# Optimization experiments

Measured on AMD Instinct MI355X. Metric: run time of the kernel, lower is better.

The kernel has to match this reference:

```python
import jax, jax.numpy as jnp
import numpy as np

K = 4
TEMPERATURE = 34.0
OUT_CH = 256
KSIZE = 3
PAD = 1


def setup_inputs() -> dict:
    key = jax.random.key(0)
    ks = jax.random.split(key, 6)
    B, C, H, W = 16, 256, 56, 56
    hidden = int(C * 0.25) + 1  # 65
    x = jax.random.normal(ks[0], (B, C, H, W), dtype=jnp.float32)
    w_fc1 = jax.random.normal(ks[1], (hidden, C), dtype=jnp.float32) * (2.0 / C) ** 0.5
    w_fc2 = jax.random.normal(ks[2], (K, hidden), dtype=jnp.float32) * (2.0 / hidden) ** 0.5
    b_fc2 = jnp.zeros((K,), dtype=jnp.float32)
    weight = jax.random.normal(ks[3], (OUT_CH, C, KSIZE, KSIZE), dtype=jnp.float32) * 0.05
    bias = jax.random.normal(ks[4], (K, OUT_CH), dtype=jnp.float32) * 0.01
    return {"x": x, "w_fc1": w_fc1, "w_fc2": w_fc2, "b_fc2": b_fc2,
            "weight": weight, "bias": bias}


def _attention(x, w_fc1, w_fc2, b_fc2):
    pooled = x.mean(axis=(2, 3))                     # [B, C] adaptive avgpool(1)
    h = jax.nn.relu(pooled @ w_fc1.T)                # 1x1 conv == linear
    raw = h @ w_fc2.T + b_fc2                        # [B, K]
    # gradient_approximation: hard one-hot fwd, softmax(x/T) bwd (straight-through)
    hard = jax.nn.one_hot(jnp.argmax(raw, axis=1), raw.shape[1], dtype=raw.dtype)
    soft = jax.nn.softmax(raw / TEMPERATURE, axis=1)
    att = jax.lax.stop_gradient(hard - soft) + soft
    return att, raw


def _quantize_banks(weight):
    # WDoReFaQuantizer with 'modified' scheme, bits 2..K+1, STE on the round step
    w = weight.reshape(-1)
    t = jnp.tanh(w)
    xq = t / jnp.max(jnp.abs(t))
    xq = (xq + 1.0) * 0.5                            # in [0, 1]
    banks = []
    for bit in range(2, 2 + K):
        a = float(1 << bit)
        q = jnp.minimum(jnp.floor(a * xq), a - 1.0) / a
        q = jax.lax.stop_gradient(q - xq) + xq       # STE: identity backward
        banks.append(q * 2.0 - 1.0)
    return jnp.stack(banks)                          # [K, O*C*k*k]


def reference(x, w_fc1, w_fc2, b_fc2, weight, bias):
    B, C, H, W = x.shape
    att, raw = _attention(x, w_fc1, w_fc2, b_fc2)    # [B, K], [B, K]
    wq = _quantize_banks(weight)                     # [K, N]
    agg_w = (att @ wq).reshape(B, OUT_CH, C, KSIZE, KSIZE)
    agg_b = att @ bias                               # [B, OUT_CH]

    def conv1(xi, wi):  # xi: [C,H,W], wi: [O,C,k,k]
        return jax.lax.conv_general_dilated(
            xi[None], wi, window_strides=(1, 1),
            padding=[(PAD, PAD), (PAD, PAD)],
            dimension_numbers=("NCHW", "OIHW", "NCHW"))[0]

    out = jax.vmap(conv1)(x, agg_w) + agg_b[:, :, None, None]
    return (out, raw)
```

## Files before the change

kernel.cpp:

```cpp
#include <hip/hip_runtime.h>
#include <math.h>

#define NB 16
#define NC 256
#define NH 56
#define NW 56
#define NHW 3136
#define NHID 65
#define NK 4
#define NOC 256
#define WN 589824
#define OUT0 12845056

#define WS_POOLED 0
#define WS_KB     4096
#define WS_MAX    4112
#define WS_MAXP   4128
#define WS_WQF    8192
#define WQB_OFF   32768ul
#define XP_OFF    4751360ul
#define WS_NEED   32325632ul

typedef unsigned int u32;
typedef unsigned short u16;
typedef unsigned long long u64;
typedef __attribute__((ext_vector_type(8))) short s8v;
typedef __attribute__((ext_vector_type(16))) float f16v;

__device__ __forceinline__ u16 f2bf(float f) {
    union { float f; u32 u; } v; v.f = f;
    u32 u = v.u;
    return (u16)((u + 0x7fffu + ((u >> 16) & 1u)) >> 16);
}

__device__ __forceinline__ void gload_lds16(const void* g, void* l) {
    __builtin_amdgcn_global_load_lds((const __attribute__((address_space(1))) u32*)g,
                                     (__attribute__((address_space(3))) u32*)l, 16, 0, 0);
}


__global__ __launch_bounds__(256) void k_prep(const float* __restrict__ x,
                                              const float* __restrict__ w,
                                              float* __restrict__ ws,
                                              float* __restrict__ scratch) {
    const int tid = threadIdx.x;
    if (blockIdx.x >= 896) {
        int j = blockIdx.x - 896;
        float m = 0.f;
        for (int i = j * 256 + tid; i < WN; i += 65536)
            m = fmaxf(m, fabsf(tanhf(w[i])));
        for (int off = 32; off > 0; off >>= 1) m = fmaxf(m, __shfl_down(m, off, 64));
        __shared__ float part[4];
        int lane = tid & 63, wv = tid >> 6;
        if (lane == 0) part[wv] = m;
        __syncthreads();
        if (tid == 0)
            ws[WS_MAXP + j] = fmaxf(fmaxf(part[0], part[1]), fmaxf(part[2], part[3]));
        return;
    }
    const int by = blockIdx.x;
    const int b = by / 56, y = by % 56;
    const int c16 = tid >> 4, q = tid & 15;
    __shared__ __align__(8) u16 Lbt[56 * 264];
    __shared__ float pl[256];
    u16* xp = (u16*)((char*)ws + XP_OFF);

    #pragma unroll
    for (int ci = 0; ci < 16; ++ci) {
        int c = ci * 16 + c16;
        float4 v = make_float4(0.f, 0.f, 0.f, 0.f);
        if (q < 14) {
            v = *(const float4*)(x + ((size_t)(b * 256 + c)) * NHW + (size_t)y * 56 + q * 4);
            Lbt[(q * 4 + 0) * 264 + c] = f2bf(v.x);
            Lbt[(q * 4 + 1) * 264 + c] = f2bf(v.y);
            Lbt[(q * 4 + 2) * 264 + c] = f2bf(v.z);
            Lbt[(q * 4 + 3) * 264 + c] = f2bf(v.w);
        }
        float s = v.x + v.y + v.z + v.w;
        s += __shfl_down(s, 8, 16);
        s += __shfl_down(s, 4, 16);
        s += __shfl_down(s, 2, 16);
        s += __shfl_down(s, 1, 16);
        if (q == 0) pl[c] = s;
    }
    __syncthreads();
    scratch[(size_t)by * 256 + tid] = pl[tid];
    u64* rowp = (u64*)xp + (size_t)(b * 58 + y + 1) * (58 * 64);
    for (int idx = tid; idx < 58 * 64; idx += 256) {
        int col = idx >> 6, cp = idx & 63;
        u64 v = 0ull;
        if (col >= 1 && col <= 56)
            v = *(const u64*)(Lbt + (col - 1) * 264 + cp * 4);
        rowp[idx] = v;
    }
    if (y == 0 || y == 55) {
        int row = (y == 0) ? 0 : 57;
        u64* brow = (u64*)xp + (size_t)(b * 58 + row) * (58 * 64);
        for (int idx = tid; idx < 58 * 64; idx += 256) brow[idx] = 0ull;
    }
}

__global__ __launch_bounds__(256) void k_mid(const float* __restrict__ w_fc1,
                                             const float* __restrict__ w_fc2,
                                             const float* __restrict__ b_fc2,
                                             const float* __restrict__ w,
                                             float* __restrict__ ws,
                                             const float* __restrict__ scratch,
                                             float* __restrict__ out_raw) {
    const int tid = threadIdx.x;
    if (blockIdx.x < 16) {
        const int b = blockIdx.x;
        __shared__ float pl[NC];
        __shared__ float hs[NHID];
        __shared__ float raws[NK];
        float p = 0.f;
        for (int y = 0; y < 56; ++y)
            p += scratch[((size_t)(b * 56 + y)) * 256 + tid];
        pl[tid] = p * (1.0f / NHW);
        __syncthreads();
        if (tid < NHID) {
            float s = 0.f;
            for (int c = 0; c < NC; ++c) s = fmaf(pl[c], w_fc1[tid * NC + c], s);
            hs[tid] = fmaxf(s, 0.f);
        }
        __syncthreads();
        if (tid < NK) {
            float s = b_fc2[tid];
            for (int j = 0; j < NHID; ++j) s = fmaf(hs[j], w_fc2[tid * NHID + j], s);
            raws[tid] = s;
            out_raw[b * NK + tid] = s;
        }
        __syncthreads();
        if (tid == 0) {
            int best = 0;
            for (int k = 1; k < NK; ++k) if (raws[k] > raws[best]) best = k;
            ((int*)(ws + WS_KB))[b] = best;
        }
        return;
    }
    __shared__ float mred[4];
    float mv = ws[WS_MAXP + tid];
    for (int off = 32; off > 0; off >>= 1) mv = fmaxf(mv, __shfl_down(mv, off, 64));
    if ((tid & 63) == 0) mred[tid >> 6] = mv;
    __syncthreads();
    const float maxt = fmaxf(fmaxf(mred[0], mred[1]), fmaxf(mred[2], mred[3]));

    u16* wqp = (u16*)((char*)ws + WQB_OFF);
    int idx = (blockIdx.x - 16) * 256 + tid;
    int o = idx >> 7, c2 = idx & 127;
    int ch0 = c2 * 2;
    int cs = ch0 >> 5, cc = ch0 & 31;
    int ks2 = cc >> 4, hf = (cc >> 3) & 1, j = cc & 7;
    int n = o & 31, ot = o >> 5;
    const float* wp = w + ((size_t)o * 256 + ch0) * 9;
    float t0[9], t1[9];
    #pragma unroll
    for (int t = 0; t < 9; ++t) t0[t] = tanhf(wp[t]);
    #pragma unroll
    for (int t = 0; t < 9; ++t) t1[t] = tanhf(wp[9 + t]);
    #pragma unroll
    for (int bank = 0; bank < 4; ++bank) {
        float a = (float)(4 << bank);
        #pragma unroll
        for (int tap = 0; tap < 9; ++tap) {
            float xq0 = (t0[tap] / maxt + 1.f) * 0.5f;
            float xq1 = (t1[tap] / maxt + 1.f) * 0.5f;
            float q0 = fminf(floorf(a * xq0), a - 1.f) / a * 2.f - 1.f;
            float q1 = fminf(floorf(a * xq1), a - 1.f) / a * 2.f - 1.f;
            u32 pk = (u32)f2bf(q0) | ((u32)f2bf(q1) << 16);
            size_t off16 = ((((size_t)((bank * 8 + ot) * 8 + cs)) * 18 + tap * 2 + ks2) * 64
                            + hf * 32 + n) * 8 + j;
            *(u32*)(wqp + off16) = pk;
        }
    }
}

__global__ __launch_bounds__(256, 2) void k_conv_mfma(const float* __restrict__ bias,
                                                      const float* __restrict__ ws_f,
                                                      float* __restrict__ out) {
    const int L = blockIdx.x;
    const int xcd = L & 7, slot = L >> 3;
    const int oq = slot >> 4;
    const int pair = xcd * 16 + (slot & 15);
    const int b = pair >> 3, strip = pair & 7;
    const int r0 = strip * 7;
    const int tid = threadIdx.x;
    const int wv = tid >> 6, lane = tid & 63;
    const int n = lane & 31, hf = lane >> 5;
    const int vw = (wv + (slot & 3)) & 3;
    const int nt = (vw == 0) ? 4 : 3;
    const int t0 = (vw == 0) ? 0 : 4 + (vw - 1) * 3;
    const int kb = ((const int*)(ws_f + WS_KB))[b];
    const u16* wqp = (const u16*)((const char*)ws_f + WQB_OFF);
    const u16* xp  = (const u16*)((const char*)ws_f + XP_OFF);

    __shared__ __align__(16) u16 Xl[2][9216];
    __shared__ __align__(16) u16 Al[2][9216];

    int bofs[4];
    #pragma unroll
    for (int t = 0; t < 4; ++t) {
        int p = (t0 + t) * 32 + n;
        if (t >= nt || p > 391) p = 391;
        int pr = p / 56, pc = p - pr * 56;
        bofs[t] = pr * 2048 + hf * 1024 + pc * 16;
    }
    const int colc = (lane < 58) ? lane : 57;
    const u16* xsrc = xp + (((size_t)(b * 58 + r0)) * 58 + colc) * 256;
    const u16* ab0 = wqp + (size_t)((kb * 8 + oq * 2 + 0) * 8) * (18 * 64 * 8);
    const u16* ab1 = wqp + (size_t)((kb * 8 + oq * 2 + 1) * 8) * (18 * 64 * 8);

    f16v acc0[4], acc1[4];
    #pragma unroll
    for (int t = 0; t < 4; ++t) { acc0[t] = (f16v)0.f; acc1[t] = (f16v)0.f; }

#define STAGE(stn, bn)                                                                   \
    {                                                                                    \
        const int csn = (stn) >> 1, ksn = (stn) & 1;                                     \
        _Pragma("unroll")                                                                \
        for (int i = 0; i < 9; ++i) {                                                    \
            int seg = wv * 9 + i;                                                        \
            if (seg < 18) {                                                              \
                gload_lds16(xsrc + (size_t)(seg >> 1) * (58 * 256) + (stn) * 16 + (seg & 1) * 8, \
                            (void*)(&Xl[bn][seg * 512]));                                \
            } else {                                                                     \
                int aa = seg - 18;                                                       \
                int tile = (aa >= 9) ? 1 : 0;                                            \
                int tap = aa - tile * 9;                                                 \
                const u16* ab = tile ? ab1 : ab0;                                        \
                gload_lds16(ab + (size_t)(csn * 18 + tap * 2 + ksn) * 512 + lane * 8,    \
                            (void*)(&Al[bn][aa * 512]));                                 \
            }                                                                            \
        }                                                                                \
    }

    STAGE(0, 0);

    #pragma unroll 1
    for (int st = 0; st < 16; ++st) {
        int pb = st & 1;
        if (st < 15) {
            STAGE(st + 1, pb ^ 1);
            asm volatile("s_waitcnt vmcnt(9)" ::: "memory");
        } else {
            asm volatile("s_waitcnt vmcnt(0)" ::: "memory");
        }
        __builtin_amdgcn_s_barrier();
        __builtin_amdgcn_s_setprio(1);
        const u16* AB = &Al[pb][0];
        const char* XB = (const char*)&Xl[pb][0];
        #pragma unroll
        for (int tap = 0; tap < 9; ++tap) {
            s8v a0 = *(const s8v*)(AB + tap * 512 + lane * 8);
            s8v a1 = *(const s8v*)(AB + (9 + tap) * 512 + lane * 8);
            const int r = tap / 3, s = tap % 3;
            const int coff = r * 2048 + s * 16;
            #pragma unroll
            for (int t = 0; t < 4; ++t)
                if (t < nt) {
                    s8v bf = *(const s8v*)(XB + bofs[t] + coff);
                    acc0[t] = __builtin_amdgcn_mfma_f32_32x32x16_bf16(a0, bf, acc0[t], 0, 0, 0);
                    acc1[t] = __builtin_amdgcn_mfma_f32_32x32x16_bf16(a1, bf, acc1[t], 0, 0, 0);
                }
        }
        __builtin_amdgcn_s_setprio(0);
        asm volatile("" ::: "memory");
        __builtin_amdgcn_s_barrier();
    }
#undef STAGE

    #pragma unroll
    for (int t = 0; t < 4; ++t)
        if (t < nt) {
            int p = (t0 + t) * 32 + n;
            if (p < 392) {
                int pr = p / 56, pc = p - pr * 56;
                float* op = out + (size_t)b * 256 * NHW + (size_t)(r0 + pr) * 56 + pc;
                #pragma unroll
                for (int reg = 0; reg < 16; ++reg) {
                    int m = (reg & 3) + 8 * (reg >> 2) + 4 * hf;
                    int o0 = oq * 64 + m;
                    op[(size_t)o0 * NHW] = acc0[t][reg] + bias[kb * NOC + o0];
                    op[(size_t)(o0 + 32) * NHW] = acc1[t][reg] + bias[kb * NOC + o0 + 32];
                }
            }
        }
}


__global__ __launch_bounds__(256) void k_pool(const float* __restrict__ x,
                                              float* __restrict__ ws) {
    int plane = blockIdx.x;
    const float* p = x + (size_t)plane * NHW;
    float s = 0.f;
    for (int i = threadIdx.x; i < NHW; i += 256) s += p[i];
    for (int off = 32; off > 0; off >>= 1) s += __shfl_down(s, off, 64);
    __shared__ float part[4];
    int lane = threadIdx.x & 63, wv = threadIdx.x >> 6;
    if (lane == 0) part[wv] = s;
    __syncthreads();
    if (threadIdx.x == 0)
        ws[WS_POOLED + plane] = part[0] + part[1] + part[2] + part[3];
}

__global__ __launch_bounds__(256) void k_fc(const float* __restrict__ w_fc1,
                                            const float* __restrict__ w_fc2,
                                            const float* __restrict__ b_fc2,
                                            float* __restrict__ ws,
                                            float* __restrict__ out_raw) {
    __shared__ float pl[NB * NC];
    __shared__ float hs[NB][NHID];
    __shared__ float raws[NB][NK];
    for (int i = threadIdx.x; i < NB * NC; i += 256)
        pl[i] = ws[WS_POOLED + i] * (1.0f / NHW);
    __syncthreads();
    for (int idx = threadIdx.x; idx < NB * NHID; idx += 256) {
        int b = idx / NHID, j = idx % NHID;
        float s = 0.f;
        for (int c = 0; c < NC; ++c) s = fmaf(pl[b * NC + c], w_fc1[j * NC + c], s);
        hs[b][j] = fmaxf(s, 0.f);
    }
    __syncthreads();
    if (threadIdx.x < NB * NK) {
        int b = threadIdx.x / NK, k = threadIdx.x % NK;
        float s = b_fc2[k];
        for (int j = 0; j < NHID; ++j) s = fmaf(hs[b][j], w_fc2[k * NHID + j], s);
        raws[b][k] = s;
        out_raw[b * NK + k] = s;
    }
    __syncthreads();
    if (threadIdx.x < NB) {
        int best = 0;
        for (int k = 1; k < NK; ++k)
            if (raws[threadIdx.x][k] > raws[threadIdx.x][best]) best = k;
        ((int*)(ws + WS_KB))[threadIdx.x] = best;
    }
}

__global__ __launch_bounds__(256) void k_maxtanh(const float* __restrict__ w,
                                                 float* __restrict__ ws) {
    float m = 0.f;
    for (int i = blockIdx.x * 256 + threadIdx.x; i < WN; i += gridDim.x * 256)
        m = fmaxf(m, fabsf(tanhf(w[i])));
    for (int off = 32; off > 0; off >>= 1) m = fmaxf(m, __shfl_down(m, off, 64));
    __shared__ float part[4];
    int lane = threadIdx.x & 63, wv = threadIdx.x >> 6;
    if (lane == 0) part[wv] = m;
    __syncthreads();
    if (threadIdx.x == 0) {
        float t = fmaxf(fmaxf(part[0], part[1]), fmaxf(part[2], part[3]));
        atomicMax((unsigned int*)ws + WS_MAX, __float_as_uint(t));
    }
}

__global__ __launch_bounds__(256) void k_quant(const float* __restrict__ w,
                                               float* __restrict__ ws) {
    float maxt = __uint_as_float(((const unsigned int*)ws)[WS_MAX]);
    float* wqf = ws + WS_WQF;
    for (int i = blockIdx.x * 256 + threadIdx.x; i < WN; i += gridDim.x * 256) {
        float t = tanhf(w[i]);
        float xq = (t / maxt + 1.0f) * 0.5f;
        #pragma unroll
        for (int k = 0; k < NK; ++k) {
            float a = (float)(4 << k);
            float q = fminf(floorf(a * xq), a - 1.0f) / a;
            wqf[(size_t)k * WN + i] = q * 2.0f - 1.0f;
        }
    }
}

__global__ __launch_bounds__(256) void k_conv(const float* __restrict__ x,
                                              const float* __restrict__ bias,
                                              const float* __restrict__ ws,
                                              float* __restrict__ out) {
    const int o_base = blockIdx.x * 16;
    const int row_base = blockIdx.y * 7;
    const int b = blockIdx.z;
    const int tid = threadIdx.x;
    const int w = tid & 63;
    const int og = tid >> 6;
    const int wc = (w < 56) ? w : 55;
    const int kb = ((const int*)(ws + WS_KB))[b];
    const float* wqf = ws + WS_WQF + (size_t)kb * WN;

    __shared__ float Xl[8][9][58];
    __shared__ float Wl[16][72];

    float acc[4][7];
    #pragma unroll
    for (int i = 0; i < 4; ++i)
        #pragma unroll
        for (int j = 0; j < 7; ++j) acc[i][j] = 0.f;

    for (int c0 = 0; c0 < NC; c0 += 8) {
        for (int idx = tid; idx < 1152; idx += 256) {
            int o = idx / 72, rem = idx - o * 72;
            Wl[o][rem] = wqf[(size_t)(o_base + o) * 2304 + c0 * 9 + rem];
        }
        for (int idx = tid; idx < 4176; idx += 256) {
            int c = idx / 522, rem = idx - c * 522;
            int ly = rem / 58, lx = rem - ly * 58;
            int gy = row_base - 1 + ly, gx = lx - 1;
            float v = 0.f;
            if (gy >= 0 && gy < NH && (unsigned)gx < (unsigned)NW)
                v = x[(((size_t)b * NC + c0 + c) * NH + gy) * NW + gx];
            Xl[c][ly][lx] = v;
        }
        __syncthreads();
        #pragma unroll 1
        for (int c = 0; c < 8; ++c) {
            float xv[9][3];
            #pragma unroll
            for (int ly = 0; ly < 9; ++ly)
                #pragma unroll
                for (int s = 0; s < 3; ++s)
                    xv[ly][s] = Xl[c][ly][wc + s];
            float wvv[4][9];
            #pragma unroll
            for (int i = 0; i < 4; ++i)
                #pragma unroll
                for (int t = 0; t < 9; ++t)
                    wvv[i][t] = Wl[og * 4 + i][c * 9 + t];
            #pragma unroll
            for (int i = 0; i < 4; ++i)
                #pragma unroll
                for (int j = 0; j < 7; ++j)
                    #pragma unroll
                    for (int r = 0; r < 3; ++r)
                        #pragma unroll
                        for (int s = 0; s < 3; ++s)
                            acc[i][j] = fmaf(wvv[i][r * 3 + s], xv[j + r][s], acc[i][j]);
        }
        __syncthreads();
    }

    if (w < 56) {
        #pragma unroll
        for (int i = 0; i < 4; ++i) {
            int o = o_base + og * 4 + i;
            float bb = bias[kb * NOC + o];
            #pragma unroll
            for (int j = 0; j < 7; ++j)
                out[(((size_t)b * NOC + o) * NH + (row_base + j)) * NW + w] = acc[i][j] + bb;
        }
    }
}

extern "C" void kernel_launch(void* const* d_in, const int* in_sizes, int n_in,
                              void* d_out, int out_size, void* d_ws, size_t ws_size,
                              hipStream_t stream) {
    const float* x      = (const float*)d_in[0];
    const float* w_fc1  = (const float*)d_in[1];
    const float* w_fc2  = (const float*)d_in[2];
    const float* b_fc2  = (const float*)d_in[3];
    const float* weight = (const float*)d_in[4];
    const float* bias   = (const float*)d_in[5];
    float* out = (float*)d_out;
    float* ws  = (float*)d_ws;

    if (ws_size >= WS_NEED) {
        hipLaunchKernelGGL(k_prep, dim3(1152), dim3(256), 0, stream, x, weight, ws, out);
        hipLaunchKernelGGL(k_mid, dim3(144), dim3(256), 0, stream,
                           w_fc1, w_fc2, b_fc2, weight, ws, out, out + OUT0);
        hipLaunchKernelGGL(k_conv_mfma, dim3(512), dim3(256), 0, stream, bias, ws, out);
    } else {
        hipLaunchKernelGGL(k_pool, dim3(NB * NC), dim3(256), 0, stream, x, ws);
        hipLaunchKernelGGL(k_fc, dim3(1), dim3(256), 0, stream,
                           w_fc1, w_fc2, b_fc2, ws, out + OUT0);
        hipLaunchKernelGGL(k_maxtanh, dim3(256), dim3(256), 0, stream, weight, ws);
        hipLaunchKernelGGL(k_quant, dim3(512), dim3(256), 0, stream, weight, ws);
        hipLaunchKernelGGL(k_conv, dim3(16, 8, NB), dim3(256), 0, stream, x, bias, ws, out);
    }
}
```

Baseline: 183.4 us.

## Interleave next-stage LDS prefetch with tap groups and batch LDS reads before MFMAs

The per-stage global-to-LDS prefetch is split into three smaller groups, each issued just before one of three tap groups of the MFMA loop, instead of all at once. Inside each tap group the A and B fragments for three taps are loaded from LDS up front, followed by one lgkmcnt wait and a sched_barrier, and then the MFMAs run back to back. The aim is to spread memory traffic more evenly across the compute and to stop LDS reads from stalling individual MFMAs. In exchange there are three barriers per stage instead of two, and more fragment registers are live at once, which may raise register pressure.

```diff
diff --git a/kernel.cpp b/kernel.cpp
--- a/kernel.cpp
+++ b/kernel.cpp
@@ -214,12 +214,12 @@
     #pragma unroll
     for (int t = 0; t < 4; ++t) { acc0[t] = (f16v)0.f; acc1[t] = (f16v)0.f; }
 
-#define STAGE(stn, bn)                                                                   \
+#define STAGE3(stn, bn, gg)                                                              \
     {                                                                                    \
         const int csn = (stn) >> 1, ksn = (stn) & 1;                                     \
         _Pragma("unroll")                                                                \
-        for (int i = 0; i < 9; ++i) {                                                    \
-            int seg = wv * 9 + i;                                                        \
+        for (int i = 0; i < 3; ++i) {                                                    \
+            int seg = wv * 9 + (gg) * 3 + i;                                             \
             if (seg < 18) {                                                              \
                 gload_lds16(xsrc + (size_t)(seg >> 1) * (58 * 256) + (stn) * 16 + (seg & 1) * 8, \
                             (void*)(&Xl[bn][seg * 512]));                                \
@@ -234,40 +234,53 @@
         }                                                                                \
     }
 
-    STAGE(0, 0);
+    STAGE3(0, 0, 0); STAGE3(0, 0, 1); STAGE3(0, 0, 2);
 
     #pragma unroll 1
     for (int st = 0; st < 16; ++st) {
         int pb = st & 1;
+        const u16* AB = &Al[pb][0];
+        const char* XB = (const char*)&Xl[pb][0];
         if (st < 15) {
-            STAGE(st + 1, pb ^ 1);
-            asm volatile("s_waitcnt vmcnt(9)" ::: "memory");
+            STAGE3(st + 1, pb ^ 1, 0);
+            asm volatile("s_waitcnt vmcnt(3)" ::: "memory");
         } else {
             asm volatile("s_waitcnt vmcnt(0)" ::: "memory");
         }
         __builtin_amdgcn_s_barrier();
-        __builtin_amdgcn_s_setprio(1);
-        const u16* AB = &Al[pb][0];
-        const char* XB = (const char*)&Xl[pb][0];
+
         #pragma unroll
-        for (int tap = 0; tap < 9; ++tap) {
-            s8v a0 = *(const s8v*)(AB + tap * 512 + lane * 8);
-            s8v a1 = *(const s8v*)(AB + (9 + tap) * 512 + lane * 8);
-            const int r = tap / 3, s = tap % 3;
-            const int coff = r * 2048 + s * 16;
-            #pragma unroll
-            for (int t = 0; t < 4; ++t)
-                if (t < nt) {
-                    s8v bf = *(const s8v*)(XB + bofs[t] + coff);
-                    acc0[t] = __builtin_amdgcn_mfma_f32_32x32x16_bf16(a0, bf, acc0[t], 0, 0, 0);
-                    acc1[t] = __builtin_amdgcn_mfma_f32_32x32x16_bf16(a1, bf, acc1[t], 0, 0, 0);
-                }
-        }
-        __builtin_amdgcn_s_setprio(0);
-        asm volatile("" ::: "memory");
-        __builtin_amdgcn_s_barrier();
-    }
-#undef STAGE
+        for (int tg = 0; tg < 3; ++tg) {
+            if (tg > 0 && st < 15) STAGE3(st + 1, pb ^ 1, tg);
+            s8v a0r[3], a1r[3], bfr[3][4];
+            #pragma unroll
+            for (int j = 0; j < 3; ++j) {
+                const int tap = tg * 3 + j;
+                a0r[j] = *(const s8v*)(AB + tap * 512 + lane * 8);
+                a1r[j] = *(const s8v*)(AB + (9 + tap) * 512 + lane * 8);
+                const int coff = (tap / 3) * 2048 + (tap % 3) * 16;
+                #pragma unroll
+                for (int t = 0; t < 4; ++t)
+                    if (t < nt)
+                        bfr[j][t] = *(const s8v*)(XB + bofs[t] + coff);
+            }
+            asm volatile("s_waitcnt lgkmcnt(0)" ::: "memory");
+            __builtin_amdgcn_sched_barrier(0);
+            __builtin_amdgcn_s_setprio(1);
+            #pragma unroll
+            for (int j = 0; j < 3; ++j)
+                #pragma unroll
+                for (int t = 0; t < 4; ++t)
+                    if (t < nt) {
+                        acc0[t] = __builtin_amdgcn_mfma_f32_32x32x16_bf16(a0r[j], bfr[j][t], acc0[t], 0, 0, 0);
+                        acc1[t] = __builtin_amdgcn_mfma_f32_32x32x16_bf16(a1r[j], bfr[j][t], acc1[t], 0, 0, 0);
+                    }
+            __builtin_amdgcn_s_setprio(0);
+            asm volatile("" ::: "memory");
+            __builtin_amdgcn_s_barrier();
+        }
+    }
+#undef STAGE3
 
     #pragma unroll
     for (int t = 0; t < 4; ++t)
```

Result: slower. 207.9 us (+13.3%).

## Balance conv MFMA waves to 3 tiles each and add tail blocks for remainder pixels

Applied to the files above, without the earlier changes.

Previously each block's 392-pixel strip was split into 13 32-pixel tiles over 4 waves, so one wave did 4 tiles and the others 3. Now every wave does exactly 3 tiles (384 pixels), and 64 extra blocks each compute the leftover 8 pixels per strip (the last 8 columns of row 6) for one batch and output quarter. The inner tap loop is manually software-pipelined, double-buffering LDS reads against MFMAs. The tail blocks use a simple synchronous load path with only two active waves, which adds a small serialized cost.

```diff
diff --git a/kernel.cpp b/kernel.cpp
--- a/kernel.cpp
+++ b/kernel.cpp
@@ -179,40 +179,83 @@
                                                       const float* __restrict__ ws_f,
                                                       float* __restrict__ out) {
     const int L = blockIdx.x;
+    const int tid = threadIdx.x;
+    const int wv = tid >> 6, lane = tid & 63;
+    const int n = lane & 31, hf = lane >> 5;
+    const u16* wqp = (const u16*)((const char*)ws_f + WQB_OFF);
+    const u16* xp  = (const u16*)((const char*)ws_f + XP_OFF);
+
+    __shared__ __align__(16) u16 SH[36864];
+
+    if (L >= 512) {
+        const int rb = L - 512;
+        const int b = rb >> 2, oq = rb & 3;
+        const int kb = ((const int*)(ws_f + WS_KB))[b];
+        const u16* ab0 = wqp + (size_t)((kb * 8 + oq * 2 + 0) * 8) * (18 * 64 * 8);
+        const u16* ab1 = wqp + (size_t)((kb * 8 + oq * 2 + 1) * 8) * (18 * 64 * 8);
+        const int tt = wv & 1;
+        const int jj = tt * 32 + n;
+        const int strip = jj >> 3, cc = jj & 7;
+        f16v ar0 = (f16v)0.f, ar1 = (f16v)0.f;
+        #pragma unroll 1
+        for (int st = 0; st < 16; ++st) {
+            for (int idx = tid; idx < 480; idx += 256) {
+                int s8 = idx / 60, rem = idx % 60;
+                int r = rem / 20, rem2 = rem % 20;
+                int col = rem2 >> 1, hfc = rem2 & 1;
+                *(s8v*)(SH + ((s8 * 3 + r) * 10 + col) * 16 + hfc * 8) =
+                    *(const s8v*)(xp + ((size_t)(b * 58 + s8 * 7 + 6 + r) * 58 + (48 + col)) * 256
+                                  + st * 16 + hfc * 8);
+            }
+            __syncthreads();
+            if (wv < 2) {
+                #pragma unroll
+                for (int tap = 0; tap < 9; ++tap) {
+                    const int r = tap / 3, s = tap % 3;
+                    s8v a0 = *(const s8v*)(ab0 + (size_t)((st >> 1) * 18 + tap * 2 + (st & 1)) * 512 + lane * 8);
+                    s8v a1 = *(const s8v*)(ab1 + (size_t)((st >> 1) * 18 + tap * 2 + (st & 1)) * 512 + lane * 8);
+                    s8v bf = *(const s8v*)(SH + ((strip * 3 + r) * 10 + (cc + s)) * 16 + hf * 8);
+                    ar0 = __builtin_amdgcn_mfma_f32_32x32x16_bf16(a0, bf, ar0, 0, 0, 0);
+                    ar1 = __builtin_amdgcn_mfma_f32_32x32x16_bf16(a1, bf, ar1, 0, 0, 0);
+                }
+            }
+            __syncthreads();
+        }
+        if (wv < 2) {
+            const int row = strip * 7 + 6, col = 48 + cc;
+            float* op = out + (size_t)b * 256 * NHW + (size_t)row * 56 + col;
+            #pragma unroll
+            for (int reg = 0; reg < 16; ++reg) {
+                int m = (reg & 3) + 8 * (reg >> 2) + 4 * hf;
+                int o0 = oq * 64 + m;
+                op[(size_t)o0 * NHW] = ar0[reg] + bias[kb * NOC + o0];
+                op[(size_t)(o0 + 32) * NHW] = ar1[reg] + bias[kb * NOC + o0 + 32];
+            }
+        }
+        return;
+    }
+
     const int xcd = L & 7, slot = L >> 3;
     const int oq = slot >> 4;
     const int pair = xcd * 16 + (slot & 15);
     const int b = pair >> 3, strip = pair & 7;
     const int r0 = strip * 7;
-    const int tid = threadIdx.x;
-    const int wv = tid >> 6, lane = tid & 63;
-    const int n = lane & 31, hf = lane >> 5;
-    const int vw = (wv + (slot & 3)) & 3;
-    const int nt = (vw == 0) ? 4 : 3;
-    const int t0 = (vw == 0) ? 0 : 4 + (vw - 1) * 3;
     const int kb = ((const int*)(ws_f + WS_KB))[b];
-    const u16* wqp = (const u16*)((const char*)ws_f + WQB_OFF);
-    const u16* xp  = (const u16*)((const char*)ws_f + XP_OFF);
-
-    __shared__ __align__(16) u16 Xl[2][9216];
-    __shared__ __align__(16) u16 Al[2][9216];
-
-    int bofs[4];
-    #pragma unroll
-    for (int t = 0; t < 4; ++t) {
-        int p = (t0 + t) * 32 + n;
-        if (t >= nt || p > 391) p = 391;
-        int pr = p / 56, pc = p - pr * 56;
-        bofs[t] = pr * 2048 + hf * 1024 + pc * 16;
+
+    int bofs0, bofs1, bofs2;
+    {
+        int p0 = (wv * 3 + 0) * 32 + n, p1 = p0 + 32, p2 = p0 + 64;
+        bofs0 = (p0 / 56) * 2048 + hf * 1024 + (p0 % 56) * 16;
+        bofs1 = (p1 / 56) * 2048 + hf * 1024 + (p1 % 56) * 16;
+        bofs2 = (p2 / 56) * 2048 + hf * 1024 + (p2 % 56) * 16;
     }
     const int colc = (lane < 58) ? lane : 57;
     const u16* xsrc = xp + (((size_t)(b * 58 + r0)) * 58 + colc) * 256;
     const u16* ab0 = wqp + (size_t)((kb * 8 + oq * 2 + 0) * 8) * (18 * 64 * 8);
     const u16* ab1 = wqp + (size_t)((kb * 8 + oq * 2 + 1) * 8) * (18 * 64 * 8);
 
-    f16v acc0[4], acc1[4];
-    #pragma unroll
-    for (int t = 0; t < 4; ++t) { acc0[t] = (f16v)0.f; acc1[t] = (f16v)0.f; }
+    f16v a00 = (f16v)0.f, a01 = (f16v)0.f, a02 = (f16v)0.f;
+    f16v a10 = (f16v)0.f, a11 = (f16v)0.f, a12 = (f16v)0.f;
 
 #define STAGE(stn, bn)                                                                   \
     {                                                                                    \
@@ -222,14 +265,14 @@
             int seg = wv * 9 + i;                                                        \
             if (seg < 18) {                                                              \
                 gload_lds16(xsrc + (size_t)(seg >> 1) * (58 * 256) + (stn) * 16 + (seg & 1) * 8, \
-                            (void*)(&Xl[bn][seg * 512]));                                \
+                            (void*)(SH + (bn) * 9216 + seg * 512));                      \
             } else {                                                                     \
                 int aa = seg - 18;                                                       \
                 int tile = (aa >= 9) ? 1 : 0;                                            \
                 int tap = aa - tile * 9;                                                 \
                 const u16* ab = tile ? ab1 : ab0;                                        \
                 gload_lds16(ab + (size_t)(csn * 18 + tap * 2 + ksn) * 512 + lane * 8,    \
-                            (void*)(&Al[bn][aa * 512]));                                 \
+                            (void*)(SH + 18432 + (bn) * 9216 + aa * 512));               \
             }                                                                            \
         }                                                                                \
     }
@@ -247,44 +290,58 @@
         }
         __builtin_amdgcn_s_barrier();
         __builtin_amdgcn_s_setprio(1);
-        const u16* AB = &Al[pb][0];
-        const char* XB = (const char*)&Xl[pb][0];
-        #pragma unroll
-        for (int tap = 0; tap < 9; ++tap) {
-            s8v a0 = *(const s8v*)(AB + tap * 512 + lane * 8);
-            s8v a1 = *(const s8v*)(AB + (9 + tap) * 512 + lane * 8);
-            const int r = tap / 3, s = tap % 3;
-            const int coff = r * 2048 + s * 16;
-            #pragma unroll
-            for (int t = 0; t < 4; ++t)
-                if (t < nt) {
-                    s8v bf = *(const s8v*)(XB + bofs[t] + coff);
-                    acc0[t] = __builtin_amdgcn_mfma_f32_32x32x16_bf16(a0, bf, acc0[t], 0, 0, 0);
-                    acc1[t] = __builtin_amdgcn_mfma_f32_32x32x16_bf16(a1, bf, acc1[t], 0, 0, 0);
-                }
-        }
+        const u16* AB = SH + 18432 + pb * 9216;
+        const char* XB = (const char*)(SH + pb * 9216);
+        s8v qa0A, qa1A, qb0A, qb1A, qb2A, qa0B, qa1B, qb0B, qb1B, qb2B;
+#define RD(tp, S)                                                                        \
+        qa0##S = *(const s8v*)(AB + (tp) * 512 + lane * 8);                              \
+        qa1##S = *(const s8v*)(AB + (9 + (tp)) * 512 + lane * 8);                        \
+        qb0##S = *(const s8v*)(XB + bofs0 + ((tp) / 3) * 2048 + ((tp) % 3) * 16);        \
+        qb1##S = *(const s8v*)(XB + bofs1 + ((tp) / 3) * 2048 + ((tp) % 3) * 16);        \
+        qb2##S = *(const s8v*)(XB + bofs2 + ((tp) / 3) * 2048 + ((tp) % 3) * 16);
+#define MM(S)                                                                            \
+        a00 = __builtin_amdgcn_mfma_f32_32x32x16_bf16(qa0##S, qb0##S, a00, 0, 0, 0);     \
+        a10 = __builtin_amdgcn_mfma_f32_32x32x16_bf16(qa1##S, qb0##S, a10, 0, 0, 0);     \
+        a01 = __builtin_amdgcn_mfma_f32_32x32x16_bf16(qa0##S, qb1##S, a01, 0, 0, 0);     \
+        a11 = __builtin_amdgcn_mfma_f32_32x32x16_bf16(qa1##S, qb1##S, a11, 0, 0, 0);     \
+        a02 = __builtin_amdgcn_mfma_f32_32x32x16_bf16(qa0##S, qb2##S, a02, 0, 0, 0);     \
+        a12 = __builtin_amdgcn_mfma_f32_32x32x16_bf16(qa1##S, qb2##S, a12, 0, 0, 0);
+        RD(0, A);
+        RD(1, B); MM(A);
+        RD(2, A); MM(B);
+        RD(3, B); MM(A);
+        RD(4, A); MM(B);
+        RD(5, B); MM(A);
+        RD(6, A); MM(B);
+        RD(7, B); MM(A);
+        RD(8, A); MM(B);
+        MM(A);
+#undef RD
+#undef MM
         __builtin_amdgcn_s_setprio(0);
         asm volatile("" ::: "memory");
         __builtin_amdgcn_s_barrier();
     }
 #undef STAGE
 
-    #pragma unroll
-    for (int t = 0; t < 4; ++t)
-        if (t < nt) {
-            int p = (t0 + t) * 32 + n;
-            if (p < 392) {
-                int pr = p / 56, pc = p - pr * 56;
-                float* op = out + (size_t)b * 256 * NHW + (size_t)(r0 + pr) * 56 + pc;
-                #pragma unroll
-                for (int reg = 0; reg < 16; ++reg) {
-                    int m = (reg & 3) + 8 * (reg >> 2) + 4 * hf;
-                    int o0 = oq * 64 + m;
-                    op[(size_t)o0 * NHW] = acc0[t][reg] + bias[kb * NOC + o0];
-                    op[(size_t)(o0 + 32) * NHW] = acc1[t][reg] + bias[kb * NOC + o0 + 32];
-                }
+    {
+        const int p0 = wv * 3 * 32 + n;
+        #pragma unroll
+        for (int t = 0; t < 3; ++t) {
+            const int p = p0 + t * 32;
+            const int pr = p / 56, pc = p % 56;
+            float* op = out + (size_t)b * 256 * NHW + (size_t)(r0 + pr) * 56 + pc;
+            const f16v accA = (t == 0) ? a00 : (t == 1) ? a01 : a02;
+            const f16v accB = (t == 0) ? a10 : (t == 1) ? a11 : a12;
+            #pragma unroll
+            for (int reg = 0; reg < 16; ++reg) {
+                int m = (reg & 3) + 8 * (reg >> 2) + 4 * hf;
+                int o0 = oq * 64 + m;
+                op[(size_t)o0 * NHW] = accA[reg] + bias[kb * NOC + o0];
+                op[(size_t)(o0 + 32) * NHW] = accB[reg] + bias[kb * NOC + o0 + 32];
             }
         }
+    }
 }
 
 
@@ -462,7 +519,7 @@
         hipLaunchKernelGGL(k_prep, dim3(1152), dim3(256), 0, stream, x, weight, ws, out);
         hipLaunchKernelGGL(k_mid, dim3(144), dim3(256), 0, stream,
                            w_fc1, w_fc2, b_fc2, weight, ws, out, out + OUT0);
-        hipLaunchKernelGGL(k_conv_mfma, dim3(512), dim3(256), 0, stream, bias, ws, out);
+        hipLaunchKernelGGL(k_conv_mfma, dim3(576), dim3(256), 0, stream, bias, ws, out);
     } else {
         hipLaunchKernelGGL(k_pool, dim3(NB * NC), dim3(256), 0, stream, x, ws);
         hipLaunchKernelGGL(k_fc, dim3(1), dim3(256), 0, stream,
```

Result: slower. 218.0 us (+18.9%).

## Store padded bf16 activations in channel-slab-major layout for contiguous conv loads

Applied to the files above, without the earlier changes.

The prep kernel now writes the bf16 padded input as per-16-channel slabs, each image row a contiguous 1920-byte run holding two 8-channel halves, instead of row-major rows with all 256 channels per column. The conv kernel's LDS staging loads therefore read contiguous 16-byte-per-lane spans rather than strided 512-byte-apart pieces. Top and bottom padding rows are dropped from storage and replaced by a shared zero slab selected by a branch. This aims to improve global load coalescing in the conv stage and cut the zero-row writes, at the cost of index arithmetic and a changed LDS layout that must still match the MFMA read offsets.

```diff
diff --git a/kernel.cpp b/kernel.cpp
--- a/kernel.cpp
+++ b/kernel.cpp
@@ -17,6 +17,7 @@
 #define WS_MAX    4112
 #define WS_MAXP   4128
 #define WS_WQF    8192
+#define ZSL_OFF   24576ul
 #define WQB_OFF   32768ul
 #define XP_OFF    4751360ul
 #define WS_NEED   32325632ul
@@ -61,9 +62,8 @@
     const int by = blockIdx.x;
     const int b = by / 56, y = by % 56;
     const int c16 = tid >> 4, q = tid & 15;
-    __shared__ __align__(8) u16 Lbt[56 * 264];
+    __shared__ __align__(16) u16 Lbt[56 * 264];
     __shared__ float pl[256];
-    u16* xp = (u16*)((char*)ws + XP_OFF);
 
     #pragma unroll
     for (int ci = 0; ci < 16; ++ci) {
@@ -85,18 +85,23 @@
     }
     __syncthreads();
     scratch[(size_t)by * 256 + tid] = pl[tid];
-    u64* rowp = (u64*)xp + (size_t)(b * 58 + y + 1) * (58 * 64);
-    for (int idx = tid; idx < 58 * 64; idx += 256) {
-        int col = idx >> 6, cp = idx & 63;
-        u64 v = 0ull;
-        if (col >= 1 && col <= 56)
-            v = *(const u64*)(Lbt + (col - 1) * 264 + cp * 4);
-        rowp[idx] = v;
-    }
-    if (y == 0 || y == 55) {
-        int row = (y == 0) ? 0 : 57;
-        u64* brow = (u64*)xp + (size_t)(b * 58 + row) * (58 * 64);
-        for (int idx = tid; idx < 58 * 64; idx += 256) brow[idx] = 0ull;
+
+    char* xpn = (char*)ws + XP_OFF;
+    #pragma unroll 1
+    for (int g = tid; g < 16 * 120; g += 256) {
+        int cs = g / 120, gg = g - cs * 120;
+        s8v v = (s8v)0;
+        if (gg < 116) {
+            int hf = (gg >= 58) ? 1 : 0;
+            int col = gg - hf * 58;
+            if (col >= 1 && col <= 56)
+                v = *(const s8v*)(Lbt + (col - 1) * 264 + cs * 16 + hf * 8);
+        }
+        *(s8v*)(xpn + (((size_t)cs * 16 + b) * 56 + y) * 1920 + gg * 16) = v;
+    }
+    if (by == 0) {
+        u64* z = (u64*)((char*)ws + ZSL_OFF);
+        for (int i = tid; i < 256; i += 256) z[i] = 0ull;
     }
 }
 
@@ -192,7 +197,8 @@
     const int t0 = (vw == 0) ? 0 : 4 + (vw - 1) * 3;
     const int kb = ((const int*)(ws_f + WS_KB))[b];
     const u16* wqp = (const u16*)((const char*)ws_f + WQB_OFF);
-    const u16* xp  = (const u16*)((const char*)ws_f + XP_OFF);
+    const char* xpn = (const char*)ws_f + XP_OFF;
+    const char* zsl = (const char*)ws_f + ZSL_OFF;
 
     __shared__ __align__(16) u16 Xl[2][9216];
     __shared__ __align__(16) u16 Al[2][9216];
@@ -205,8 +211,6 @@
         int pr = p / 56, pc = p - pr * 56;
         bofs[t] = pr * 2048 + hf * 1024 + pc * 16;
     }
-    const int colc = (lane < 58) ? lane : 57;
-    const u16* xsrc = xp + (((size_t)(b * 58 + r0)) * 58 + colc) * 256;
     const u16* ab0 = wqp + (size_t)((kb * 8 + oq * 2 + 0) * 8) * (18 * 64 * 8);
     const u16* ab1 = wqp + (size_t)((kb * 8 + oq * 2 + 1) * 8) * (18 * 64 * 8);
 
@@ -221,8 +225,13 @@
         for (int i = 0; i < 9; ++i) {                                                    \
             int seg = wv * 9 + i;                                                        \
             if (seg < 18) {                                                              \
-                gload_lds16(xsrc + (size_t)(seg >> 1) * (58 * 256) + (stn) * 16 + (seg & 1) * 8, \
-                            (void*)(&Xl[bn][seg * 512]));                                \
+                int row = seg >> 1, half = seg & 1;                                      \
+                int rr = r0 + row;                                                       \
+                const char* src = (rr >= 1 && rr <= 56)                                  \
+                    ? xpn + (((size_t)(stn) * 16 + b) * 56 + (rr - 1)) * 1920            \
+                    : zsl;                                                               \
+                gload_lds16(src + half * 928 + lane * 16,                                \
+                            (void*)(&Xl[bn][row * 1024 + half * 512]));                  \
             } else {                                                                     \
                 int aa = seg - 18;                                                       \
                 int tile = (aa >= 9) ? 1 : 0;                                            \
```

Result: no change. 183.2 us (-0.1%).
